# Kernel optimization log

Measured on AMD Instinct MI355X. Metric: run time of the kernel, lower is better.

## Reference

```python
import jax, jax.numpy as jnp
import numpy as np

B, N, F = 512, 2048, 64
T = 4            # number of atom types
H1, H2 = 64, 32  # hidden widths; final layer outputs 1 (per-atom energy)


def setup_inputs() -> dict:
    key = jax.random.key(0)
    ks = jax.random.split(key, 8)
    x = jax.random.normal(ks[0], (B, N, F), dtype=jnp.float32)
    atomic_numbers = jax.random.randint(ks[1], (N,), 0, T)
    s = 0.05
    # Per-type MLP parameters, stacked over the type axis (torch Linear layout: [out, in]).
    w0 = jax.random.normal(ks[2], (T, H1, F), dtype=jnp.float32) * s
    b0 = jax.random.normal(ks[3], (T, H1), dtype=jnp.float32) * s
    w1 = jax.random.normal(ks[4], (T, H2, H1), dtype=jnp.float32) * s
    b1 = jax.random.normal(ks[5], (T, H2), dtype=jnp.float32) * s
    w2 = jax.random.normal(ks[6], (T, 1, H2), dtype=jnp.float32) * s
    b2 = jax.random.normal(ks[7], (T, 1), dtype=jnp.float32) * s
    return {"x": x, "atomic_numbers": atomic_numbers,
            "w0": w0, "b0": b0, "w1": w1, "b1": b1, "w2": w2, "b2": b2}


def reference(x, atomic_numbers, w0, b0, w1, b1, w2, b2):
    # Behler-Parrinello: route each atom through the MLP of its atom type,
    # then sum per-atom energies over atoms.  The torch version gathers atoms
    # by type, runs each type's MLP, and scatters back; here we evaluate all
    # T type-MLPs batched over the type axis and select with a one-hot mask
    # (identical math, jit-friendly, no data-dependent shapes).
    onehot = jax.nn.one_hot(atomic_numbers, w0.shape[0], dtype=x.dtype)  # [N, T]
    h = jax.nn.silu(jnp.einsum('bnf,thf->tbnh', x, w0) + b0[:, None, None, :])   # [T,B,N,H1]
    h = jax.nn.silu(jnp.einsum('tbnh,tgh->tbng', h, w1) + b1[:, None, None, :])  # [T,B,N,H2]
    e = jnp.einsum('tbng,tog->tbno', h, w2) + b2[:, None, None, :]               # [T,B,N,1]
    e = e[..., 0]                                                                # [T,B,N]
    per_atom = jnp.einsum('tbn,nt->bn', e, onehot)  # select the matching type per atom
    return per_atom.sum(axis=-1)                    # [B]
```

## Files before the change

kernel.cpp:

```cpp
#include <hip/hip_runtime.h>
#include <hip/hip_bf16.h>


#define B_ 512
#define N_ 2048
#define F_ 64
#define T_ 4
#define H1_ 64
#define H2_ 32

#define BT 16
#define WAVES 4
#define NCHUNK 64
#define SLICE (NCHUNK / WAVES)

typedef __attribute__((ext_vector_type(8))) short bf16x8;
typedef __attribute__((ext_vector_type(4))) short bf16x4;
typedef __attribute__((ext_vector_type(4))) float f32x4;

__device__ inline float silu_f(float v) {
    return v * __builtin_amdgcn_rcpf(1.0f + __expf(-v));
}

__device__ inline bf16x8 pack8(float4 a, float4 b) {
    union { __hip_bfloat162 h[4]; bf16x8 v; } u;
    u.h[0] = __float22bfloat162_rn({a.x, a.y});
    u.h[1] = __float22bfloat162_rn({a.z, a.w});
    u.h[2] = __float22bfloat162_rn({b.x, b.y});
    u.h[3] = __float22bfloat162_rn({b.z, b.w});
    return u.v;
}

__device__ inline bf16x4 pack4(float a, float b, float c, float d) {
    union { __hip_bfloat162 h[2]; bf16x4 v; } u;
    u.h[0] = __float22bfloat162_rn({a, b});
    u.h[1] = __float22bfloat162_rn({c, d});
    return u.v;
}

__device__ inline float bf_at(bf16x4 v, int r) {
    union { bf16x4 v; __hip_bfloat16 h[4]; } u; u.v = v;
    return __bfloat162float(u.h[r]);
}

__global__ __launch_bounds__(256, 3) void bpnn_kernel(
    const float* __restrict__ x, const int* __restrict__ an,
    const float* __restrict__ w0, const float* __restrict__ b0,
    const float* __restrict__ w1, const float* __restrict__ b1,
    const float* __restrict__ w2, const float* __restrict__ b2,
    float* __restrict__ out)
{
    __shared__ __align__(16) __hip_bfloat16 trb[WAVES][BT][68];
    __shared__ int sidx[NCHUNK];
    __shared__ float red[BT];

    const int tid  = threadIdx.x;
    const int wave = tid >> 6;
    const int lane = tid & 63;
    const int lr   = lane & 15;
    const int q    = lane >> 4;
    const int b0i  = blockIdx.y * BT;
    const int n0   = blockIdx.x * NCHUNK;

    if (tid < BT) red[tid] = 0.0f;

    {
        const int t = an[n0 + lane];
        unsigned long long m0 = __ballot(t == 0);
        unsigned long long m1 = __ballot(t == 1);
        unsigned long long m2 = __ballot(t == 2);
        unsigned long long m3 = __ballot(t == 3);
        const int base1 = (int)__popcll(m0);
        const int base2 = base1 + (int)__popcll(m1);
        const int base3 = base2 + (int)__popcll(m2);
        const unsigned long long mb = (1ull << lane) - 1ull;
        int r;
        if (t == 0)      r = (int)__popcll(m0 & mb);
        else if (t == 1) r = base1 + (int)__popcll(m1 & mb);
        else if (t == 2) r = base2 + (int)__popcll(m2 & mb);
        else             r = base3 + (int)__popcll(m3 & mb);
        if (wave == 0) sidx[r] = (t << 8) | lane;
    }
    __syncthreads();

    const float* xb_ = x + (size_t)(b0i + lr) * (N_ * F_) + (size_t)n0 * F_ + q * 8;
    __hip_bfloat16* trbw = &trb[wave][lr][0];

    const int s0 = wave * SLICE;
    const int s1 = s0 + SLICE;

    float esum0 = 0.f, esum1 = 0.f, bsum = 0.f;

    bf16x8 aw000, aw001, aw010, aw011, aw020, aw021, aw030, aw031;
    bf16x8 aw100, aw101, aw110, aw111;
    bf16x4 b0f0, b0f1, b0f2, b0f3, b1f0, b1f1, w2f0, w2f1;
    float b2c = 0.f;

    int p = s0;
    int id0 = __builtin_amdgcn_readfirstlane(sidx[p]);
    int id1 = __builtin_amdgcn_readfirstlane(sidx[p + 1]);
    float4 sa0, sa1, sa2, sa3, sb0, sb1, sb2, sb3;
    {
        const float4* pA = reinterpret_cast<const float4*>(xb_ + (id0 & 0xFF) * F_);
        sa0 = pA[0]; sa1 = pA[1]; sa2 = pA[8]; sa3 = pA[9];
        const float4* pB = reinterpret_cast<const float4*>(xb_ + (id1 & 0xFF) * F_);
        sb0 = pB[0]; sb1 = pB[1]; sb2 = pB[8]; sb3 = pB[9];
    }

    while (p < s1) {
        const int t = id0 >> 8;
        {
            const float* wb = w0 + t * (H1_ * F_) + lr * F_ + q * 8;
            const float4* pw;
            pw = reinterpret_cast<const float4*>(wb +  0 * F_ +  0); aw000 = pack8(pw[0], pw[1]);
            pw = reinterpret_cast<const float4*>(wb +  0 * F_ + 32); aw001 = pack8(pw[0], pw[1]);
            pw = reinterpret_cast<const float4*>(wb + 16 * F_ +  0); aw010 = pack8(pw[0], pw[1]);
            pw = reinterpret_cast<const float4*>(wb + 16 * F_ + 32); aw011 = pack8(pw[0], pw[1]);
            pw = reinterpret_cast<const float4*>(wb + 32 * F_ +  0); aw020 = pack8(pw[0], pw[1]);
            pw = reinterpret_cast<const float4*>(wb + 32 * F_ + 32); aw021 = pack8(pw[0], pw[1]);
            pw = reinterpret_cast<const float4*>(wb + 48 * F_ +  0); aw030 = pack8(pw[0], pw[1]);
            pw = reinterpret_cast<const float4*>(wb + 48 * F_ + 32); aw031 = pack8(pw[0], pw[1]);
            const float* wc = w1 + t * (H2_ * H1_) + lr * H1_ + q * 8;
            pw = reinterpret_cast<const float4*>(wc +  0 * H1_ +  0); aw100 = pack8(pw[0], pw[1]);
            pw = reinterpret_cast<const float4*>(wc +  0 * H1_ + 32); aw101 = pack8(pw[0], pw[1]);
            pw = reinterpret_cast<const float4*>(wc + 16 * H1_ +  0); aw110 = pack8(pw[0], pw[1]);
            pw = reinterpret_cast<const float4*>(wc + 16 * H1_ + 32); aw111 = pack8(pw[0], pw[1]);
            float4 v;
            v = *reinterpret_cast<const float4*>(b0 + t * H1_ +  0 + q * 4); b0f0 = pack4(v.x, v.y, v.z, v.w);
            v = *reinterpret_cast<const float4*>(b0 + t * H1_ + 16 + q * 4); b0f1 = pack4(v.x, v.y, v.z, v.w);
            v = *reinterpret_cast<const float4*>(b0 + t * H1_ + 32 + q * 4); b0f2 = pack4(v.x, v.y, v.z, v.w);
            v = *reinterpret_cast<const float4*>(b0 + t * H1_ + 48 + q * 4); b0f3 = pack4(v.x, v.y, v.z, v.w);
            v = *reinterpret_cast<const float4*>(b1 + t * H2_ +  0 + q * 4); b1f0 = pack4(v.x, v.y, v.z, v.w);
            v = *reinterpret_cast<const float4*>(b1 + t * H2_ + 16 + q * 4); b1f1 = pack4(v.x, v.y, v.z, v.w);
            v = *reinterpret_cast<const float4*>(w2 + t * H2_ +  0 + q * 4); w2f0 = pack4(v.x, v.y, v.z, v.w);
            v = *reinterpret_cast<const float4*>(w2 + t * H2_ + 16 + q * 4); w2f1 = pack4(v.x, v.y, v.z, v.w);
            b2c = b2[t];
        }

        for (;;) {
            bf16x8 xf0 = pack8(sa0, sa1);
            bf16x8 xf1 = pack8(sa2, sa3);
            sa0 = sb0; sa1 = sb1; sa2 = sb2; sa3 = sb3;
            int pn = p + 2;
            int idn = id1;
            if (pn < s1) idn = __builtin_amdgcn_readfirstlane(sidx[pn]);
            {
                const float4* pB = reinterpret_cast<const float4*>(xb_ + (idn & 0xFF) * F_);
                sb0 = pB[0]; sb1 = pB[1]; sb2 = pB[8]; sb3 = pB[9];
            }
            bsum += b2c;

            f32x4 acc0 = {0.f,0.f,0.f,0.f}, acc1 = {0.f,0.f,0.f,0.f};
            f32x4 acc2 = {0.f,0.f,0.f,0.f}, acc3 = {0.f,0.f,0.f,0.f};
            acc0 = __builtin_amdgcn_mfma_f32_16x16x32_bf16(aw000, xf0, acc0, 0, 0, 0);
            acc0 = __builtin_amdgcn_mfma_f32_16x16x32_bf16(aw001, xf1, acc0, 0, 0, 0);
            acc1 = __builtin_amdgcn_mfma_f32_16x16x32_bf16(aw010, xf0, acc1, 0, 0, 0);
            acc1 = __builtin_amdgcn_mfma_f32_16x16x32_bf16(aw011, xf1, acc1, 0, 0, 0);
            acc2 = __builtin_amdgcn_mfma_f32_16x16x32_bf16(aw020, xf0, acc2, 0, 0, 0);
            acc2 = __builtin_amdgcn_mfma_f32_16x16x32_bf16(aw021, xf1, acc2, 0, 0, 0);
            acc3 = __builtin_amdgcn_mfma_f32_16x16x32_bf16(aw030, xf0, acc3, 0, 0, 0);
            acc3 = __builtin_amdgcn_mfma_f32_16x16x32_bf16(aw031, xf1, acc3, 0, 0, 0);

            {
                float v0 = silu_f(acc0[0] + bf_at(b0f0, 0));
                float v1 = silu_f(acc0[1] + bf_at(b0f0, 1));
                float v2 = silu_f(acc0[2] + bf_at(b0f0, 2));
                float v3 = silu_f(acc0[3] + bf_at(b0f0, 3));
                *reinterpret_cast<bf16x4*>(trbw +  0 + q * 4) = pack4(v0, v1, v2, v3);
                v0 = silu_f(acc1[0] + bf_at(b0f1, 0));
                v1 = silu_f(acc1[1] + bf_at(b0f1, 1));
                v2 = silu_f(acc1[2] + bf_at(b0f1, 2));
                v3 = silu_f(acc1[3] + bf_at(b0f1, 3));
                *reinterpret_cast<bf16x4*>(trbw + 16 + q * 4) = pack4(v0, v1, v2, v3);
                v0 = silu_f(acc2[0] + bf_at(b0f2, 0));
                v1 = silu_f(acc2[1] + bf_at(b0f2, 1));
                v2 = silu_f(acc2[2] + bf_at(b0f2, 2));
                v3 = silu_f(acc2[3] + bf_at(b0f2, 3));
                *reinterpret_cast<bf16x4*>(trbw + 32 + q * 4) = pack4(v0, v1, v2, v3);
                v0 = silu_f(acc3[0] + bf_at(b0f3, 0));
                v1 = silu_f(acc3[1] + bf_at(b0f3, 1));
                v2 = silu_f(acc3[2] + bf_at(b0f3, 2));
                v3 = silu_f(acc3[3] + bf_at(b0f3, 3));
                *reinterpret_cast<bf16x4*>(trbw + 48 + q * 4) = pack4(v0, v1, v2, v3);
            }
            __builtin_amdgcn_wave_barrier();

            bf16x8 hb0 = *reinterpret_cast<const bf16x8*>(trbw + q * 8);
            bf16x8 hb1 = *reinterpret_cast<const bf16x8*>(trbw + 32 + q * 8);
            __builtin_amdgcn_wave_barrier();

            f32x4 acB0 = {0.f,0.f,0.f,0.f}, acB1 = {0.f,0.f,0.f,0.f};
            acB0 = __builtin_amdgcn_mfma_f32_16x16x32_bf16(aw100, hb0, acB0, 0, 0, 0);
            acB0 = __builtin_amdgcn_mfma_f32_16x16x32_bf16(aw101, hb1, acB0, 0, 0, 0);
            acB1 = __builtin_amdgcn_mfma_f32_16x16x32_bf16(aw110, hb0, acB1, 0, 0, 0);
            acB1 = __builtin_amdgcn_mfma_f32_16x16x32_bf16(aw111, hb1, acB1, 0, 0, 0);

#pragma unroll
            for (int r = 0; r < 4; ++r) {
                esum0 += silu_f(acB0[r] + bf_at(b1f0, r)) * bf_at(w2f0, r);
                esum1 += silu_f(acB1[r] + bf_at(b1f1, r)) * bf_at(w2f1, r);
            }

            ++p;
            id0 = id1; id1 = idn;
            if (p >= s1 || (id0 >> 8) != t) break;
        }
    }

    float esum = esum0 + esum1;
    esum += __shfl_xor(esum, 16);
    esum += __shfl_xor(esum, 32);
    if (q == 0) atomicAdd(&red[lr], esum + bsum);
    __syncthreads();
    if (tid < BT) atomicAdd(&out[b0i + tid], red[tid]);
}

extern "C" void kernel_launch(void* const* d_in, const int* in_sizes, int n_in,
                              void* d_out, int out_size, void* d_ws, size_t ws_size,
                              hipStream_t stream) {
    const float* x  = (const float*)d_in[0];
    const int*   an = (const int*)d_in[1];
    const float* w0 = (const float*)d_in[2];
    const float* b0 = (const float*)d_in[3];
    const float* w1 = (const float*)d_in[4];
    const float* b1 = (const float*)d_in[5];
    const float* w2 = (const float*)d_in[6];
    const float* b2 = (const float*)d_in[7];
    float* out = (float*)d_out;

    hipMemsetAsync(out, 0, B_ * sizeof(float), stream);
    dim3 grid(N_ / NCHUNK, B_ / BT);
    bpnn_kernel<<<grid, 256, 0, stream>>>(x, an, w0, b0, w1, b1, w2, b2, out);
}
```

Before: 386.4 us.

## Stage x tiles into LDS with async global_load_lds double buffering

Replaces per-wave register prefetch of gathered atom rows with cooperative, contiguous global-to-LDS async loads of 8-atom tiles into a double-buffered shared buffer. Atoms are now sorted by type within 8-atom groups, and each wave handles two atoms per tile, reloading weights only on type change. It also drops the shared-memory reduction in favour of direct global atomics from each wave. This adds about 66KB of LDS and a block barrier per tile, and removes the occupancy hint, which may lower occupancy.

```diff
diff --git a/kernel.cpp b/kernel.cpp
--- a/kernel.cpp
+++ b/kernel.cpp
@@ -11,12 +11,17 @@
 
 #define BT 16
 #define WAVES 4
-#define NCHUNK 64
-#define SLICE (NCHUNK / WAVES)
+#define NC 8
+#define NTILE 8
+#define NCHUNK (NC * NTILE)
+#define ROWPAD 2064
 
 typedef __attribute__((ext_vector_type(8))) short bf16x8;
 typedef __attribute__((ext_vector_type(4))) short bf16x4;
 typedef __attribute__((ext_vector_type(4))) float f32x4;
+
+typedef const __attribute__((address_space(1))) void* gas_ptr;
+typedef __attribute__((address_space(3))) void* las_ptr;
 
 __device__ inline float silu_f(float v) {
     return v * __builtin_amdgcn_rcpf(1.0f + __expf(-v));
@@ -43,16 +48,16 @@
     return __bfloat162float(u.h[r]);
 }
 
-__global__ __launch_bounds__(256, 3) void bpnn_kernel(
+__global__ __launch_bounds__(256) void bpnn_kernel(
     const float* __restrict__ x, const int* __restrict__ an,
     const float* __restrict__ w0, const float* __restrict__ b0,
     const float* __restrict__ w1, const float* __restrict__ b1,
     const float* __restrict__ w2, const float* __restrict__ b2,
     float* __restrict__ out)
 {
+    __shared__ __align__(16) char xbuf[2][BT * ROWPAD];
     __shared__ __align__(16) __hip_bfloat16 trb[WAVES][BT][68];
     __shared__ int sidx[NCHUNK];
-    __shared__ float red[BT];
 
     const int tid  = threadIdx.x;
     const int wave = tid >> 6;
@@ -62,32 +67,43 @@
     const int b0i  = blockIdx.y * BT;
     const int n0   = blockIdx.x * NCHUNK;
 
-    if (tid < BT) red[tid] = 0.0f;
-
     {
         const int t = an[n0 + lane];
         unsigned long long m0 = __ballot(t == 0);
         unsigned long long m1 = __ballot(t == 1);
         unsigned long long m2 = __ballot(t == 2);
         unsigned long long m3 = __ballot(t == 3);
-        const int base1 = (int)__popcll(m0);
-        const int base2 = base1 + (int)__popcll(m1);
-        const int base3 = base2 + (int)__popcll(m2);
-        const unsigned long long mb = (1ull << lane) - 1ull;
-        int r;
-        if (t == 0)      r = (int)__popcll(m0 & mb);
-        else if (t == 1) r = base1 + (int)__popcll(m1 & mb);
-        else if (t == 2) r = base2 + (int)__popcll(m2 & mb);
-        else             r = base3 + (int)__popcll(m3 & mb);
-        if (wave == 0) sidx[r] = (t << 8) | lane;
+        const int g = lane >> 3, j = lane & 7;
+        const unsigned gm0 = (unsigned)(m0 >> (g * 8)) & 0xFFu;
+        const unsigned gm1 = (unsigned)(m1 >> (g * 8)) & 0xFFu;
+        const unsigned gm2 = (unsigned)(m2 >> (g * 8)) & 0xFFu;
+        const unsigned gm3 = (unsigned)(m3 >> (g * 8)) & 0xFFu;
+        const unsigned gmt = (t == 0) ? gm0 : (t == 1) ? gm1 : (t == 2) ? gm2 : gm3;
+        int below = 0;
+        if (t > 0) below += (int)__popc(gm0);
+        if (t > 1) below += (int)__popc(gm1);
+        if (t > 2) below += (int)__popc(gm2);
+        const int pos = (g << 3) + below + (int)__popc(gmt & ((1u << j) - 1u));
+        if (wave == 0) sidx[pos] = (t << 8) | j;
     }
+
+    const char* xB = (const char*)x;
+    auto stage = [&](int pb, int c) {
+#pragma unroll
+        for (int rr = 0; rr < 4; ++rr) {
+            const int rw = (wave << 2) + rr;
+            const char* g = xB
+                + ((size_t)(b0i + rw) * (N_ * F_) + (size_t)(n0 + c * NC) * F_) * 4
+                + (size_t)lane * 16;
+            char* l = &xbuf[pb][rw * ROWPAD];
+            __builtin_amdgcn_global_load_lds((gas_ptr)g,          (las_ptr)l,          16, 0, 0);
+            __builtin_amdgcn_global_load_lds((gas_ptr)(g + 1024), (las_ptr)(l + 1024), 16, 0, 0);
+        }
+    };
+
+    stage(0, 0);
     __syncthreads();
-
-    const float* xb_ = x + (size_t)(b0i + lr) * (N_ * F_) + (size_t)n0 * F_ + q * 8;
-    __hip_bfloat16* trbw = &trb[wave][lr][0];
-
-    const int s0 = wave * SLICE;
-    const int s1 = s0 + SLICE;
+    const int myid = sidx[lane];
 
     float esum0 = 0.f, esum1 = 0.f, bsum = 0.f;
 
@@ -95,59 +111,57 @@
     bf16x8 aw100, aw101, aw110, aw111;
     bf16x4 b0f0, b0f1, b0f2, b0f3, b1f0, b1f1, w2f0, w2f1;
     float b2c = 0.f;
-
-    int p = s0;
-    int id0 = __builtin_amdgcn_readfirstlane(sidx[p]);
-    int id1 = __builtin_amdgcn_readfirstlane(sidx[p + 1]);
-    float4 sa0, sa1, sa2, sa3, sb0, sb1, sb2, sb3;
-    {
-        const float4* pA = reinterpret_cast<const float4*>(xb_ + (id0 & 0xFF) * F_);
-        sa0 = pA[0]; sa1 = pA[1]; sa2 = pA[8]; sa3 = pA[9];
-        const float4* pB = reinterpret_cast<const float4*>(xb_ + (id1 & 0xFF) * F_);
-        sb0 = pB[0]; sb1 = pB[1]; sb2 = pB[8]; sb3 = pB[9];
-    }
-
-    while (p < s1) {
-        const int t = id0 >> 8;
-        {
-            const float* wb = w0 + t * (H1_ * F_) + lr * F_ + q * 8;
-            const float4* pw;
-            pw = reinterpret_cast<const float4*>(wb +  0 * F_ +  0); aw000 = pack8(pw[0], pw[1]);
-            pw = reinterpret_cast<const float4*>(wb +  0 * F_ + 32); aw001 = pack8(pw[0], pw[1]);
-            pw = reinterpret_cast<const float4*>(wb + 16 * F_ +  0); aw010 = pack8(pw[0], pw[1]);
-            pw = reinterpret_cast<const float4*>(wb + 16 * F_ + 32); aw011 = pack8(pw[0], pw[1]);
-            pw = reinterpret_cast<const float4*>(wb + 32 * F_ +  0); aw020 = pack8(pw[0], pw[1]);
-            pw = reinterpret_cast<const float4*>(wb + 32 * F_ + 32); aw021 = pack8(pw[0], pw[1]);
-            pw = reinterpret_cast<const float4*>(wb + 48 * F_ +  0); aw030 = pack8(pw[0], pw[1]);
-            pw = reinterpret_cast<const float4*>(wb + 48 * F_ + 32); aw031 = pack8(pw[0], pw[1]);
-            const float* wc = w1 + t * (H2_ * H1_) + lr * H1_ + q * 8;
-            pw = reinterpret_cast<const float4*>(wc +  0 * H1_ +  0); aw100 = pack8(pw[0], pw[1]);
-            pw = reinterpret_cast<const float4*>(wc +  0 * H1_ + 32); aw101 = pack8(pw[0], pw[1]);
-            pw = reinterpret_cast<const float4*>(wc + 16 * H1_ +  0); aw110 = pack8(pw[0], pw[1]);
-            pw = reinterpret_cast<const float4*>(wc + 16 * H1_ + 32); aw111 = pack8(pw[0], pw[1]);
-            float4 v;
-            v = *reinterpret_cast<const float4*>(b0 + t * H1_ +  0 + q * 4); b0f0 = pack4(v.x, v.y, v.z, v.w);
-            v = *reinterpret_cast<const float4*>(b0 + t * H1_ + 16 + q * 4); b0f1 = pack4(v.x, v.y, v.z, v.w);
-            v = *reinterpret_cast<const float4*>(b0 + t * H1_ + 32 + q * 4); b0f2 = pack4(v.x, v.y, v.z, v.w);
-            v = *reinterpret_cast<const float4*>(b0 + t * H1_ + 48 + q * 4); b0f3 = pack4(v.x, v.y, v.z, v.w);
-            v = *reinterpret_cast<const float4*>(b1 + t * H2_ +  0 + q * 4); b1f0 = pack4(v.x, v.y, v.z, v.w);
-            v = *reinterpret_cast<const float4*>(b1 + t * H2_ + 16 + q * 4); b1f1 = pack4(v.x, v.y, v.z, v.w);
-            v = *reinterpret_cast<const float4*>(w2 + t * H2_ +  0 + q * 4); w2f0 = pack4(v.x, v.y, v.z, v.w);
-            v = *reinterpret_cast<const float4*>(w2 + t * H2_ + 16 + q * 4); w2f1 = pack4(v.x, v.y, v.z, v.w);
-            b2c = b2[t];
-        }
-
-        for (;;) {
-            bf16x8 xf0 = pack8(sa0, sa1);
-            bf16x8 xf1 = pack8(sa2, sa3);
-            sa0 = sb0; sa1 = sb1; sa2 = sb2; sa3 = sb3;
-            int pn = p + 2;
-            int idn = id1;
-            if (pn < s1) idn = __builtin_amdgcn_readfirstlane(sidx[pn]);
-            {
-                const float4* pB = reinterpret_cast<const float4*>(xb_ + (idn & 0xFF) * F_);
-                sb0 = pB[0]; sb1 = pB[1]; sb2 = pB[8]; sb3 = pB[9];
+    int cur_t = -1;
+
+    __hip_bfloat16* trbw = &trb[wave][lr][0];
+
+#pragma unroll 1
+    for (int c = 0; c < NTILE; ++c) {
+        const int pb = c & 1;
+        if (c + 1 < NTILE) stage(pb ^ 1, c + 1);
+
+#pragma unroll
+        for (int jj = 0; jj < 2; ++jj) {
+            const int id = __builtin_amdgcn_readlane(myid, (c << 3) + (wave << 1) + jj);
+            const int t    = id >> 8;
+            const int nloc = id & 0xFF;
+            if (t != cur_t) {
+                cur_t = t;
+                const float* wb = w0 + t * (H1_ * F_) + lr * F_ + q * 8;
+                const float4* pw;
+                pw = reinterpret_cast<const float4*>(wb +  0 * F_ +  0); aw000 = pack8(pw[0], pw[1]);
+                pw = reinterpret_cast<const float4*>(wb +  0 * F_ + 32); aw001 = pack8(pw[0], pw[1]);
+                pw = reinterpret_cast<const float4*>(wb + 16 * F_ +  0); aw010 = pack8(pw[0], pw[1]);
+                pw = reinterpret_cast<const float4*>(wb + 16 * F_ + 32); aw011 = pack8(pw[0], pw[1]);
+                pw = reinterpret_cast<const float4*>(wb + 32 * F_ +  0); aw020 = pack8(pw[0], pw[1]);
+                pw = reinterpret_cast<const float4*>(wb + 32 * F_ + 32); aw021 = pack8(pw[0], pw[1]);
+                pw = reinterpret_cast<const float4*>(wb + 48 * F_ +  0); aw030 = pack8(pw[0], pw[1]);
+                pw = reinterpret_cast<const float4*>(wb + 48 * F_ + 32); aw031 = pack8(pw[0], pw[1]);
+                const float* wc = w1 + t * (H2_ * H1_) + lr * H1_ + q * 8;
+                pw = reinterpret_cast<const float4*>(wc +  0 * H1_ +  0); aw100 = pack8(pw[0], pw[1]);
+                pw = reinterpret_cast<const float4*>(wc +  0 * H1_ + 32); aw101 = pack8(pw[0], pw[1]);
+                pw = reinterpret_cast<const float4*>(wc + 16 * H1_ +  0); aw110 = pack8(pw[0], pw[1]);
+                pw = reinterpret_cast<const float4*>(wc + 16 * H1_ + 32); aw111 = pack8(pw[0], pw[1]);
+                float4 v;
+                v = *reinterpret_cast<const float4*>(b0 + t * H1_ +  0 + q * 4); b0f0 = pack4(v.x, v.y, v.z, v.w);
+                v = *reinterpret_cast<const float4*>(b0 + t * H1_ + 16 + q * 4); b0f1 = pack4(v.x, v.y, v.z, v.w);
+                v = *reinterpret_cast<const float4*>(b0 + t * H1_ + 32 + q * 4); b0f2 = pack4(v.x, v.y, v.z, v.w);
+                v = *reinterpret_cast<const float4*>(b0 + t * H1_ + 48 + q * 4); b0f3 = pack4(v.x, v.y, v.z, v.w);
+                v = *reinterpret_cast<const float4*>(b1 + t * H2_ +  0 + q * 4); b1f0 = pack4(v.x, v.y, v.z, v.w);
+                v = *reinterpret_cast<const float4*>(b1 + t * H2_ + 16 + q * 4); b1f1 = pack4(v.x, v.y, v.z, v.w);
+                v = *reinterpret_cast<const float4*>(w2 + t * H2_ +  0 + q * 4); w2f0 = pack4(v.x, v.y, v.z, v.w);
+                v = *reinterpret_cast<const float4*>(w2 + t * H2_ + 16 + q * 4); w2f1 = pack4(v.x, v.y, v.z, v.w);
+                b2c = b2[t];
             }
+
+            const char* rb = &xbuf[pb][lr * ROWPAD + nloc * 256 + q * 32];
+            float4 f0 = *reinterpret_cast<const float4*>(rb);
+            float4 f1 = *reinterpret_cast<const float4*>(rb + 16);
+            float4 f2 = *reinterpret_cast<const float4*>(rb + 128);
+            float4 f3 = *reinterpret_cast<const float4*>(rb + 144);
+
+            bf16x8 xf0 = pack8(f0, f1);
+            bf16x8 xf1 = pack8(f2, f3);
             bsum += b2c;
 
             f32x4 acc0 = {0.f,0.f,0.f,0.f}, acc1 = {0.f,0.f,0.f,0.f};
@@ -200,19 +214,15 @@
                 esum0 += silu_f(acB0[r] + bf_at(b1f0, r)) * bf_at(w2f0, r);
                 esum1 += silu_f(acB1[r] + bf_at(b1f1, r)) * bf_at(w2f1, r);
             }
-
-            ++p;
-            id0 = id1; id1 = idn;
-            if (p >= s1 || (id0 >> 8) != t) break;
         }
+
+        __syncthreads();
     }
 
     float esum = esum0 + esum1;
     esum += __shfl_xor(esum, 16);
     esum += __shfl_xor(esum, 32);
-    if (q == 0) atomicAdd(&red[lr], esum + bsum);
-    __syncthreads();
-    if (tid < BT) atomicAdd(&out[b0i + tid], red[tid]);
+    if (q == 0) atomicAdd(&out[b0i + lr], esum + bsum);
 }
 
 extern "C" void kernel_launch(void* const* d_in, const int* in_sizes, int n_in,
```

New measurement: 444.2 us. 1.15x slower.
